# Performance work log

Hardware: AMD Instinct MI355X
Metric: run time of the kernel (lower is better)

Reference implementation:

```python
import jax, jax.numpy as jnp
import numpy as np

C = 256
HEADS = 8
HEAD_DIM = C // HEADS
SCALE = HEAD_DIM ** -0.5
POOL = 2
LN_EPS = 1e-5


def setup_inputs() -> dict:
    key = jax.random.key(0)
    ks = jax.random.split(key, 10)
    B, H, W = 8, 64, 64
    std = 0.02
    return {
        "x": jax.random.normal(ks[0], (B, C, H, W), jnp.float32),
        "Wq": jax.random.normal(ks[1], (HEADS, C), jnp.float32) * std,
        "Wk": jax.random.normal(ks[2], (HEADS, C), jnp.float32) * std,
        "Wv": jax.random.normal(ks[3], (C, C), jnp.float32) * std,
        "Wsr": jax.random.normal(ks[4], (C, C), jnp.float32) * (2.0 / C) ** 0.5,
        "bsr": jnp.zeros((C,), jnp.float32),
        "gamma": jnp.ones((C,), jnp.float32),
        "beta": jnp.zeros((C,), jnp.float32),
        "Wp": jax.random.normal(ks[5], (C, C), jnp.float32) * std,
        "bp": jnp.zeros((C,), jnp.float32),
    }


def reference(x, Wq, Wk, Wv, Wsr, bsr, gamma, beta, Wp, bp):
    B, Cc, H, W = x.shape
    N = H * W
    # tokens [B, N, C]
    tok = x.reshape(B, Cc, N).transpose(0, 2, 1)
    # q: Linear(C -> heads), per-head scalar query  [B, heads, N]
    q = jnp.einsum("bnc,hc->bhn", tok, Wq)
    # spatial reduction: avgpool(pool_ratio) then 1x1 conv
    xp = x.reshape(B, Cc, H // POOL, POOL, W // POOL, POOL).mean(axis=(3, 5))
    xs = jnp.einsum("bchw,oc->bohw", xp, Wsr) + bsr[None, :, None, None]
    M = (H // POOL) * (W // POOL)
    x_ = xs.reshape(B, Cc, M).transpose(0, 2, 1)  # [B, M, C]
    # LayerNorm + GELU (exact erf, torch default)
    mu = x_.mean(-1, keepdims=True)
    var = ((x_ - mu) ** 2).mean(-1, keepdims=True)
    x_ = (x_ - mu) * jax.lax.rsqrt(var + LN_EPS) * gamma + beta
    x_ = jax.nn.gelu(x_, approximate=False)
    # k: per-head scalar key [B, heads, M]; v: [B, heads, M, head_dim]
    k = jnp.einsum("bmc,hc->bhm", x_, Wk)
    v = jnp.einsum("bmc,oc->bmo", x_, Wv).reshape(B, M, HEADS, HEAD_DIM).transpose(0, 2, 1, 3)
    # rank-1 attention scores [B, heads, N, M]
    attn = jax.nn.softmax(q[:, :, :, None] * k[:, :, None, :] * SCALE, axis=-1)
    out = jnp.einsum("bhnm,bhmd->bhnd", attn, v)  # [B, heads, N, head_dim]
    out = out.transpose(0, 2, 1, 3).reshape(B, N, Cc)
    out = out @ Wp.T + bp
    return out.transpose(0, 2, 1).reshape(B, Cc, H, W)
```

## Files before the change

### kernel.cpp

```cpp
#include <hip/hip_runtime.h>
#include <math.h>


#define NH 8
#define NJ 8
#define NT (NH * NJ)
#define SCALE 0.17677669529663687f

__device__ __constant__ float INVFACT[NJ] = {
    1.0f, 1.0f, 0.5f, 1.6666666666666666e-01f, 4.1666666666666664e-02f,
    8.3333333333333332e-03f, 1.3888888888888889e-03f, 1.9841269841269841e-04f};

__global__ void k0_q_prep(const float* __restrict__ x, const float* __restrict__ Wq,
                          const float* __restrict__ Wsr, const float* __restrict__ Wv,
                          float* __restrict__ q01, float* __restrict__ WsrT,
                          float* __restrict__ WvT) {
    __shared__ float wq[NH * 128];
    const int tid = threadIdx.x;
    const int blk = blockIdx.x;
    if (blk < 256) {
        const int b = blk >> 5, half = (blk >> 4) & 1, nt = blk & 15;
#pragma unroll
        for (int r = 0; r < 4; ++r) {
            int idx = r * 256 + tid;
            int h = idx >> 7, cc = idx & 127;
            wq[idx] = Wq[h * 256 + half * 128 + cc];
        }
        __syncthreads();
        const int n = nt * 256 + tid;
        const float* xb = x + (((size_t)b << 8) + half * 128) * 4096 + n;
        float acc[NH] = {};
#pragma unroll 8
        for (int c = 0; c < 128; ++c) {
            float xv = xb[(size_t)c << 12];
#pragma unroll
            for (int h = 0; h < NH; ++h) acc[h] += xv * wq[h * 128 + c];
        }
#pragma unroll
        for (int h = 0; h < NH; ++h)
            q01[((size_t)(half * 64 + b * 8 + h) << 12) + n] = acc[h];
    } else {
        const float* W = (blk < 288) ? Wsr : Wv;
        float* WT = (blk < 288) ? WsrT : WvT;
        const int c0 = (blk & 31) * 8;
#pragma unroll
        for (int r = 0; r < 2; ++r) {
            int fidx = r * 256 + tid;
            int c = c0 + (fidx >> 6), o4 = (fidx & 63) * 4;
            float4 t;
            t.x = W[(size_t)(o4 + 0) * 256 + c];
            t.y = W[(size_t)(o4 + 1) * 256 + c];
            t.z = W[(size_t)(o4 + 2) * 256 + c];
            t.w = W[(size_t)(o4 + 3) * 256 + c];
            *(float4*)&WT[(size_t)c * 256 + o4] = t;
        }
    }
}

__global__ void ka_mega(const float* __restrict__ x, const float* __restrict__ WsrT,
                        const float* __restrict__ bsr, const float* __restrict__ WvT,
                        const float* __restrict__ gamma, const float* __restrict__ beta,
                        const float* __restrict__ Wk,
                        float* __restrict__ v, float* __restrict__ kout) {
    __shared__ float smem[20352];
    float* a_pool = smem;
    float* wpan   = smem + 1152;
    float* g_lds  = smem + 9472;
    float4* wkv   = (float4*)(smem + 17792);
    float4* glv   = (float4*)(smem + 19840);
    float4* blv   = (float4*)(smem + 20096);

    const int tid = threadIdx.x;
    const int blk = blockIdx.x;
    const int b = blk >> 5, mt = blk & 31;
    const int m0 = mt * 32;
    const int i2 = mt;

    const int ccs = tid >> 3, jg = tid & 7;
    const int mg = tid & 7, og = tid >> 3;

    const float4* Wk4 = (const float4*)Wk;
    wkv[tid] = Wk4[tid];
    wkv[256 + tid] = Wk4[256 + tid];
    if (tid < 64) {
        glv[tid] = ((const float4*)gamma)[tid];
        blv[tid] = ((const float4*)beta)[tid];
    }

    float acc[4][8] = {};
    for (int c0 = 0; c0 < 256; c0 += 32) {
        __syncthreads();
        {
            const float* p = x + ((size_t)(b * 256 + c0 + ccs) << 12) +
                             i2 * 128 + jg * 8;
            float4 r00 = *(const float4*)p;
            float4 r01 = *(const float4*)(p + 4);
            float4 r10 = *(const float4*)(p + 64);
            float4 r11 = *(const float4*)(p + 68);
            float4 pv;
            pv.x = 0.25f * ((r00.x + r00.y) + (r10.x + r10.y));
            pv.y = 0.25f * ((r00.z + r00.w) + (r10.z + r10.w));
            pv.z = 0.25f * ((r01.x + r01.y) + (r11.x + r11.y));
            pv.w = 0.25f * ((r01.z + r01.w) + (r11.z + r11.w));
            *(float4*)&a_pool[ccs * 36 + jg * 4] = pv;
        }
#pragma unroll
        for (int r = 0; r < 8; ++r) {
            int fidx = r * 256 + tid;
            int cc = fidx >> 6, o4 = (fidx & 63) * 4;
            *(float4*)&wpan[cc * 260 + o4] =
                *(const float4*)&WsrT[(size_t)(c0 + cc) * 256 + o4];
        }
        __syncthreads();
#pragma unroll
        for (int cc = 0; cc < 32; ++cc) {
            float4 av = *(const float4*)&a_pool[cc * 36 + mg * 4];
            float4 b0 = *(const float4*)&wpan[cc * 260 + og * 8];
            float4 b1 = *(const float4*)&wpan[cc * 260 + og * 8 + 4];
            float am[4] = {av.x, av.y, av.z, av.w};
            float bo[8] = {b0.x, b0.y, b0.z, b0.w, b1.x, b1.y, b1.z, b1.w};
#pragma unroll
            for (int i = 0; i < 4; ++i)
#pragma unroll
                for (int j = 0; j < 8; ++j) acc[i][j] += am[i] * bo[j];
        }
    }
    {
        float4 bs0 = *(const float4*)&bsr[og * 8];
        float4 bs1 = *(const float4*)&bsr[og * 8 + 4];
#pragma unroll
        for (int i = 0; i < 4; ++i) {
            float4 w0, w1;
            w0.x = acc[i][0] + bs0.x; w0.y = acc[i][1] + bs0.y;
            w0.z = acc[i][2] + bs0.z; w0.w = acc[i][3] + bs0.w;
            w1.x = acc[i][4] + bs1.x; w1.y = acc[i][5] + bs1.y;
            w1.z = acc[i][6] + bs1.z; w1.w = acc[i][7] + bs1.w;
            *(float4*)&g_lds[(mg * 4 + i) * 260 + og * 8] = w0;
            *(float4*)&g_lds[(mg * 4 + i) * 260 + og * 8 + 4] = w1;
        }
    }
    __syncthreads();

    const int wave = tid >> 6, lane = tid & 63;
    const float4 g4 = glv[lane], be4 = blv[lane];
#pragma unroll
    for (int ti = 0; ti < 8; ++ti) {
        const int mm = wave * 8 + ti;
        float4 vv = *(const float4*)&g_lds[mm * 260 + lane * 4];
        float s = (vv.x + vv.y) + (vv.z + vv.w);
        float s2 = (vv.x * vv.x + vv.y * vv.y) + (vv.z * vv.z + vv.w * vv.w);
#pragma unroll
        for (int off = 1; off < 64; off <<= 1) {
            s += __shfl_xor(s, off);
            s2 += __shfl_xor(s2, off);
        }
        const float mu = s * (1.f / 256.f);
        const float rstd = rsqrtf(s2 * (1.f / 256.f) - mu * mu + 1e-5f);
        float4 gg;
        {
            float xh;
            xh = (vv.x - mu) * rstd * g4.x + be4.x;
            gg.x = 0.5f * xh * (1.f + erff(xh * 0.70710678118654752f));
            xh = (vv.y - mu) * rstd * g4.y + be4.y;
            gg.y = 0.5f * xh * (1.f + erff(xh * 0.70710678118654752f));
            xh = (vv.z - mu) * rstd * g4.z + be4.z;
            gg.z = 0.5f * xh * (1.f + erff(xh * 0.70710678118654752f));
            xh = (vv.w - mu) * rstd * g4.w + be4.w;
            gg.w = 0.5f * xh * (1.f + erff(xh * 0.70710678118654752f));
        }
        *(float4*)&g_lds[mm * 260 + lane * 4] = gg;
        float acck[NH];
#pragma unroll
        for (int h = 0; h < NH; ++h) {
            float4 w = wkv[h * 64 + lane];
            acck[h] = (gg.x * w.x + gg.y * w.y) + (gg.z * w.z + gg.w * w.w);
        }
#pragma unroll
        for (int off = 1; off < 64; off <<= 1)
#pragma unroll
            for (int h = 0; h < NH; ++h) acck[h] += __shfl_xor(acck[h], off);
        if (lane == 0) {
#pragma unroll
            for (int h = 0; h < NH; ++h)
                kout[((size_t)(b * 8 + h) << 10) + m0 + mm] = acck[h];
        }
    }

    float accv[4][8] = {};
    for (int c0 = 0; c0 < 256; c0 += 32) {
        __syncthreads();
#pragma unroll
        for (int r = 0; r < 8; ++r) {
            int fidx = r * 256 + tid;
            int cc = fidx >> 6, o4 = (fidx & 63) * 4;
            *(float4*)&wpan[cc * 260 + o4] =
                *(const float4*)&WvT[(size_t)(c0 + cc) * 256 + o4];
        }
        __syncthreads();
#pragma unroll
        for (int cc = 0; cc < 32; ++cc) {
            const int c = c0 + cc;
            float a0 = g_lds[(mg * 4 + 0) * 260 + c];
            float a1 = g_lds[(mg * 4 + 1) * 260 + c];
            float a2 = g_lds[(mg * 4 + 2) * 260 + c];
            float a3 = g_lds[(mg * 4 + 3) * 260 + c];
            float4 b0 = *(const float4*)&wpan[cc * 260 + og * 8];
            float4 b1 = *(const float4*)&wpan[cc * 260 + og * 8 + 4];
            float bo[8] = {b0.x, b0.y, b0.z, b0.w, b1.x, b1.y, b1.z, b1.w};
#pragma unroll
            for (int j = 0; j < 8; ++j) {
                accv[0][j] += a0 * bo[j];
                accv[1][j] += a1 * bo[j];
                accv[2][j] += a2 * bo[j];
                accv[3][j] += a3 * bo[j];
            }
        }
    }
#pragma unroll
    for (int i = 0; i < 4; ++i) {
        float4 r0, r1;
        r0.x = accv[i][0]; r0.y = accv[i][1]; r0.z = accv[i][2]; r0.w = accv[i][3];
        r1.x = accv[i][4]; r1.y = accv[i][5]; r1.z = accv[i][6]; r1.w = accv[i][7];
        float* dst = &v[((size_t)(b << 10) + m0 + mg * 4 + i) * 256 + og * 8];
        *(float4*)dst = r0;
        *(float4*)(dst + 4) = r1;
    }
}

__global__ void kc_moments_project(const float* __restrict__ kin,
                                   const float* __restrict__ v,
                                   const float* __restrict__ Wp,
                                   float* __restrict__ P, float* __restrict__ S2) {
    const int bh = blockIdx.x;
    const int h = bh & 7, b = bh >> 3;
    const int tid = threadIdx.x;
    const int g = tid >> 5, d = tid & 31;
    float accM[NJ] = {};
    float accS[NJ] = {};
    const float* kb = kin + ((size_t)bh << 10);
    const float* vb = v + ((size_t)b << 18) + h * 32 + d;
#pragma unroll 4
    for (int mi = 0; mi < 128; ++mi) {
        int m = g * 128 + mi;
        float km = kb[m];
        float w = vb[(size_t)m << 8];
        float t = w, ts = 1.f;
#pragma unroll
        for (int j = 0; j < NJ; ++j) {
            accM[j] += t;
            accS[j] += ts;
            t *= km;
            ts *= km;
        }
    }
    __shared__ float red[8][NJ][33];
#pragma unroll
    for (int j = 0; j < NJ; ++j) red[g][j][d] = accM[j];
    if (d == 0) {
#pragma unroll
        for (int j = 0; j < NJ; ++j) red[g][j][32] = accS[j];
    }
    __syncthreads();
    __shared__ float Ms[NJ][33];
    for (int idx = tid; idx < NJ * 33; idx += 256) {
        int j = idx / 33, dd = idx % 33;
        float sum = 0.f;
#pragma unroll
        for (int gg = 0; gg < 8; ++gg) sum += red[gg][j][dd];
        Ms[j][dd] = sum * INVFACT[j];
    }
    __syncthreads();
    const int c = tid;
    float wp[32];
    const float* wrow = Wp + c * 256 + h * 32;
#pragma unroll
    for (int i = 0; i < 8; ++i) {
        float4 t = *(const float4*)(wrow + i * 4);
        wp[i * 4 + 0] = t.x; wp[i * 4 + 1] = t.y;
        wp[i * 4 + 2] = t.z; wp[i * 4 + 3] = t.w;
    }
#pragma unroll
    for (int j = 0; j < NJ; ++j) {
        float s = 0.f;
#pragma unroll
        for (int dd = 0; dd < 32; ++dd) s += wp[dd] * Ms[j][dd];
        P[((size_t)bh * NJ + j) * 256 + c] = s;
    }
    if (tid < NJ) S2[bh * NJ + tid] = Ms[tid][32];
}

__global__ void kd_out(const float* __restrict__ q01, const float* __restrict__ S2,
                       const float* __restrict__ P, const float* __restrict__ bp,
                       float* __restrict__ out) {
    __shared__ float p_lds[NT * 264];
    __shared__ float coef_lds[NT * 32];
    __shared__ float s2l[NT];
    const int tid = threadIdx.x;
    const int b = blockIdx.x >> 7, nt = blockIdx.x & 127;
    const int n0 = nt * 32;
    if (tid < NT) s2l[tid] = S2[b * NT + tid];
    const float* Pb = P + (size_t)b * (NT * 256);
#pragma unroll
    for (int r = 0; r < 16; ++r) {
        int fidx = r * 256 + tid;
        int t = fidx >> 6, c4 = (fidx & 63) * 4;
        *(float4*)&p_lds[t * 264 + c4] = *(const float4*)&Pb[t * 256 + c4];
    }
    __syncthreads();
    {
        const int n = tid & 31, h = tid >> 5;
        size_t qi = ((size_t)(b * NH + h) << 12) + n0 + n;
        float a = (q01[qi] + q01[qi + ((size_t)64 << 12)]) * SCALE;
        float den = s2l[h * NJ + NJ - 1];
#pragma unroll
        for (int j = NJ - 2; j >= 0; --j) den = den * a + s2l[h * NJ + j];
        float p = 1.0f / den;
#pragma unroll
        for (int j = 0; j < NJ; ++j) {
            coef_lds[(h * NJ + j) * 32 + n] = p;
            p *= a;
        }
    }
    __syncthreads();
    const int ng = tid & 7, og = tid >> 3;
    float acc[8][4] = {};
#pragma unroll 8
    for (int t = 0; t < NT; ++t) {
        float4 nv = *(const float4*)&coef_lds[t * 32 + ng * 4];
        float4 cv0 = *(const float4*)&p_lds[t * 264 + og * 8];
        float4 cv1 = *(const float4*)&p_lds[t * 264 + og * 8 + 4];
        float nm[4] = {nv.x, nv.y, nv.z, nv.w};
        float cm[8] = {cv0.x, cv0.y, cv0.z, cv0.w, cv1.x, cv1.y, cv1.z, cv1.w};
#pragma unroll
        for (int i = 0; i < 8; ++i)
#pragma unroll
            for (int j = 0; j < 4; ++j) acc[i][j] += cm[i] * nm[j];
    }
    float* ob = out + ((size_t)(b << 8) + og * 8) * 4096 + n0 + ng * 4;
#pragma unroll
    for (int i = 0; i < 8; ++i) {
        float bpc = bp[og * 8 + i];
        float4 r;
        r.x = acc[i][0] + bpc; r.y = acc[i][1] + bpc;
        r.z = acc[i][2] + bpc; r.w = acc[i][3] + bpc;
        *(float4*)(ob + (size_t)i * 4096) = r;
    }
}

extern "C" void kernel_launch(void* const* d_in, const int* in_sizes, int n_in,
                              void* d_out, int out_size, void* d_ws, size_t ws_size,
                              hipStream_t stream) {
    const float* x     = (const float*)d_in[0];
    const float* Wq    = (const float*)d_in[1];
    const float* Wk    = (const float*)d_in[2];
    const float* Wv    = (const float*)d_in[3];
    const float* Wsr   = (const float*)d_in[4];
    const float* bsr   = (const float*)d_in[5];
    const float* gamma = (const float*)d_in[6];
    const float* beta  = (const float*)d_in[7];
    const float* Wp    = (const float*)d_in[8];
    const float* bp    = (const float*)d_in[9];
    float* out = (float*)d_out;

    float* ws   = (float*)d_ws;
    float* vbuf = ws;
    float* q01  = vbuf + 2097152;
    float* kbuf = q01 + 524288;
    float* P    = kbuf + 65536;
    float* S2   = P + 131072;
    float* WsrT = S2 + 512;
    float* WvT  = WsrT + 65536;

    k0_q_prep<<<320, 256, 0, stream>>>(x, Wq, Wsr, Wv, q01, WsrT, WvT);
    ka_mega<<<256, 256, 0, stream>>>(x, WsrT, bsr, WvT, gamma, beta, Wk,
                                     vbuf, kbuf);
    kc_moments_project<<<64, 256, 0, stream>>>(kbuf, vbuf, Wp, P, S2);
    kd_out<<<1024, 256, 0, stream>>>(q01, S2, P, bp, out);
}
```

Before: 206.8 us.

## Double-buffer weight panels via registers and swizzle LDS tiles in ka_mega

Restructures ka_mega so all pooled inputs are computed up front into a swizzled LDS tile. Both GEMM stages now stream weight panels through a register-staged double buffer, which removes one barrier per iteration and overlaps global loads with FMAs. The GELU output is also written transposed and swizzled, so the second GEMM reads float4 vectors instead of scalar strided loads. LDS use rises to about 140KB with launch_bounds(256,1), which limits each CU to one block and raises register pressure.

```diff
diff --git a/kernel.cpp b/kernel.cpp
--- a/kernel.cpp
+++ b/kernel.cpp
@@ -57,18 +57,19 @@
     }
 }
 
-__global__ void ka_mega(const float* __restrict__ x, const float* __restrict__ WsrT,
-                        const float* __restrict__ bsr, const float* __restrict__ WvT,
-                        const float* __restrict__ gamma, const float* __restrict__ beta,
-                        const float* __restrict__ Wk,
-                        float* __restrict__ v, float* __restrict__ kout) {
-    __shared__ float smem[20352];
-    float* a_pool = smem;
-    float* wpan   = smem + 1152;
-    float* g_lds  = smem + 9472;
-    float4* wkv   = (float4*)(smem + 17792);
-    float4* glv   = (float4*)(smem + 19840);
-    float4* blv   = (float4*)(smem + 20096);
+__global__ __launch_bounds__(256, 1) void ka_mega(
+        const float* __restrict__ x, const float* __restrict__ WsrT,
+        const float* __restrict__ bsr, const float* __restrict__ WvT,
+        const float* __restrict__ gamma, const float* __restrict__ beta,
+        const float* __restrict__ Wk,
+        float* __restrict__ v, float* __restrict__ kout) {
+    __shared__ __attribute__((aligned(16))) float smem[35456];
+    float* wpan  = smem;
+    float* gsh   = smem + 16384;
+    float* g_t   = smem + 24704;
+    float4* wkv  = (float4*)(smem + 32896);
+    float4* glv  = (float4*)(smem + 34944);
+    float4* blv  = (float4*)(smem + 35200);
 
     const int tid = threadIdx.x;
     const int blk = blockIdx.x;
@@ -76,56 +77,74 @@
     const int m0 = mt * 32;
     const int i2 = mt;
 
-    const int ccs = tid >> 3, jg = tid & 7;
     const int mg = tid & 7, og = tid >> 3;
 
-    const float4* Wk4 = (const float4*)Wk;
-    wkv[tid] = Wk4[tid];
-    wkv[256 + tid] = Wk4[256 + tid];
-    if (tid < 64) {
-        glv[tid] = ((const float4*)gamma)[tid];
-        blv[tid] = ((const float4*)beta)[tid];
-    }
-
-    float acc[4][8] = {};
-    for (int c0 = 0; c0 < 256; c0 += 32) {
-        __syncthreads();
-        {
-            const float* p = x + ((size_t)(b * 256 + c0 + ccs) << 12) +
-                             i2 * 128 + jg * 8;
-            float4 r00 = *(const float4*)p;
-            float4 r01 = *(const float4*)(p + 4);
-            float4 r10 = *(const float4*)(p + 64);
-            float4 r11 = *(const float4*)(p + 68);
+    {
+        const int ccs = tid >> 3, jg = tid & 7;
+        const int pcb = (jg * 4) ^ (((ccs >> 2) & 7) << 2);
+#pragma unroll 2
+        for (int p = 0; p < 8; ++p) {
+            const int c = p * 32 + ccs;
+            const float* px = x + ((size_t)(b * 256 + c) << 12) + i2 * 128 + jg * 8;
+            float4 r00 = *(const float4*)px;
+            float4 r01 = *(const float4*)(px + 4);
+            float4 r10 = *(const float4*)(px + 64);
+            float4 r11 = *(const float4*)(px + 68);
             float4 pv;
             pv.x = 0.25f * ((r00.x + r00.y) + (r10.x + r10.y));
             pv.y = 0.25f * ((r00.z + r00.w) + (r10.z + r10.w));
             pv.z = 0.25f * ((r01.x + r01.y) + (r11.x + r11.y));
             pv.w = 0.25f * ((r01.z + r01.w) + (r11.z + r11.w));
-            *(float4*)&a_pool[ccs * 36 + jg * 4] = pv;
-        }
-#pragma unroll
-        for (int r = 0; r < 8; ++r) {
-            int fidx = r * 256 + tid;
-            int cc = fidx >> 6, o4 = (fidx & 63) * 4;
-            *(float4*)&wpan[cc * 260 + o4] =
-                *(const float4*)&WsrT[(size_t)(c0 + cc) * 256 + o4];
-        }
-        __syncthreads();
-#pragma unroll
-        for (int cc = 0; cc < 32; ++cc) {
-            float4 av = *(const float4*)&a_pool[cc * 36 + mg * 4];
-            float4 b0 = *(const float4*)&wpan[cc * 260 + og * 8];
-            float4 b1 = *(const float4*)&wpan[cc * 260 + og * 8 + 4];
-            float am[4] = {av.x, av.y, av.z, av.w};
-            float bo[8] = {b0.x, b0.y, b0.z, b0.w, b1.x, b1.y, b1.z, b1.w};
-#pragma unroll
-            for (int i = 0; i < 4; ++i)
-#pragma unroll
-                for (int j = 0; j < 8; ++j) acc[i][j] += am[i] * bo[j];
-        }
-    }
-    {
+            *(float4*)&gsh[(c << 5) + pcb] = pv;
+        }
+    }
+    {
+        const float4* src = (const float4*)WsrT;
+#pragma unroll
+        for (int r = 0; r < 8; ++r)
+            *(float4*)&wpan[(r * 256 + tid) * 4] = src[r * 256 + tid];
+    }
+    {
+        const float4* Wk4 = (const float4*)Wk;
+        wkv[tid] = Wk4[tid];
+        wkv[256 + tid] = Wk4[256 + tid];
+        if (tid < 64) {
+            glv[tid] = ((const float4*)gamma)[tid];
+            blv[tid] = ((const float4*)beta)[tid];
+        }
+    }
+    __syncthreads();
+
+    float4 wreg[8];
+    {
+        float acc[4][8] = {};
+        for (int p = 0; p < 8; ++p) {
+            if (p < 7) {
+                const float4* src = (const float4*)(WsrT + ((size_t)(p + 1) << 13));
+#pragma unroll
+                for (int r = 0; r < 8; ++r) wreg[r] = src[r * 256 + tid];
+            }
+            const float* wp = wpan + ((p & 1) << 13);
+#pragma unroll
+            for (int cc = 0; cc < 32; ++cc) {
+                const int swzc = ((cc >> 2) & 7) << 2;
+                float4 av = *(const float4*)&gsh[((p * 32 + cc) << 5) + ((mg << 2) ^ swzc)];
+                float4 b0 = *(const float4*)&wp[cc * 256 + og * 8];
+                float4 b1 = *(const float4*)&wp[cc * 256 + og * 8 + 4];
+                float am[4] = {av.x, av.y, av.z, av.w};
+                float bo[8] = {b0.x, b0.y, b0.z, b0.w, b1.x, b1.y, b1.z, b1.w};
+#pragma unroll
+                for (int i = 0; i < 4; ++i)
+#pragma unroll
+                    for (int j = 0; j < 8; ++j) acc[i][j] += am[i] * bo[j];
+            }
+            if (p < 7) {
+#pragma unroll
+                for (int r = 0; r < 8; ++r)
+                    *(float4*)&wpan[(((p + 1) & 1) << 13) + (r * 256 + tid) * 4] = wreg[r];
+            }
+            __syncthreads();
+        }
         float4 bs0 = *(const float4*)&bsr[og * 8];
         float4 bs1 = *(const float4*)&bsr[og * 8 + 4];
 #pragma unroll
@@ -135,86 +154,115 @@
             w0.z = acc[i][2] + bs0.z; w0.w = acc[i][3] + bs0.w;
             w1.x = acc[i][4] + bs1.x; w1.y = acc[i][5] + bs1.y;
             w1.z = acc[i][6] + bs1.z; w1.w = acc[i][7] + bs1.w;
-            *(float4*)&g_lds[(mg * 4 + i) * 260 + og * 8] = w0;
-            *(float4*)&g_lds[(mg * 4 + i) * 260 + og * 8 + 4] = w1;
+            *(float4*)&gsh[(mg * 4 + i) * 260 + og * 8] = w0;
+            *(float4*)&gsh[(mg * 4 + i) * 260 + og * 8 + 4] = w1;
         }
     }
     __syncthreads();
 
     const int wave = tid >> 6, lane = tid & 63;
-    const float4 g4 = glv[lane], be4 = blv[lane];
-#pragma unroll
-    for (int ti = 0; ti < 8; ++ti) {
-        const int mm = wave * 8 + ti;
-        float4 vv = *(const float4*)&g_lds[mm * 260 + lane * 4];
-        float s = (vv.x + vv.y) + (vv.z + vv.w);
-        float s2 = (vv.x * vv.x + vv.y * vv.y) + (vv.z * vv.z + vv.w * vv.w);
-#pragma unroll
-        for (int off = 1; off < 64; off <<= 1) {
-            s += __shfl_xor(s, off);
-            s2 += __shfl_xor(s2, off);
-        }
-        const float mu = s * (1.f / 256.f);
-        const float rstd = rsqrtf(s2 * (1.f / 256.f) - mu * mu + 1e-5f);
-        float4 gg;
+    {
+        const float4 g4 = glv[lane], be4 = blv[lane];
+        float4 wkreg[NH];
+#pragma unroll
+        for (int h = 0; h < NH; ++h) wkreg[h] = wkv[h * 64 + lane];
         {
-            float xh;
-            xh = (vv.x - mu) * rstd * g4.x + be4.x;
-            gg.x = 0.5f * xh * (1.f + erff(xh * 0.70710678118654752f));
-            xh = (vv.y - mu) * rstd * g4.y + be4.y;
-            gg.y = 0.5f * xh * (1.f + erff(xh * 0.70710678118654752f));
-            xh = (vv.z - mu) * rstd * g4.z + be4.z;
-            gg.z = 0.5f * xh * (1.f + erff(xh * 0.70710678118654752f));
-            xh = (vv.w - mu) * rstd * g4.w + be4.w;
-            gg.w = 0.5f * xh * (1.f + erff(xh * 0.70710678118654752f));
-        }
-        *(float4*)&g_lds[mm * 260 + lane * 4] = gg;
-        float acck[NH];
-#pragma unroll
-        for (int h = 0; h < NH; ++h) {
-            float4 w = wkv[h * 64 + lane];
-            acck[h] = (gg.x * w.x + gg.y * w.y) + (gg.z * w.z + gg.w * w.w);
-        }
-#pragma unroll
-        for (int off = 1; off < 64; off <<= 1)
-#pragma unroll
-            for (int h = 0; h < NH; ++h) acck[h] += __shfl_xor(acck[h], off);
-        if (lane == 0) {
-#pragma unroll
-            for (int h = 0; h < NH; ++h)
-                kout[((size_t)(b * 8 + h) << 10) + m0 + mm] = acck[h];
-        }
-    }
+            const float4* src = (const float4*)WvT;
+#pragma unroll
+            for (int r = 0; r < 8; ++r) wreg[r] = src[r * 256 + tid];
+        }
+        float4 gg4[8];
+#pragma unroll
+        for (int ti = 0; ti < 8; ++ti) {
+            const int mm = wave * 8 + ti;
+            float4 vv = *(const float4*)&gsh[mm * 260 + lane * 4];
+            float s = (vv.x + vv.y) + (vv.z + vv.w);
+            float s2 = (vv.x * vv.x + vv.y * vv.y) + (vv.z * vv.z + vv.w * vv.w);
+#pragma unroll
+            for (int off = 1; off < 64; off <<= 1) {
+                s += __shfl_xor(s, off);
+                s2 += __shfl_xor(s2, off);
+            }
+            const float mu = s * (1.f / 256.f);
+            const float rstd = rsqrtf(s2 * (1.f / 256.f) - mu * mu + 1e-5f);
+            float4 gg;
+            {
+                float xh;
+                xh = (vv.x - mu) * rstd * g4.x + be4.x;
+                gg.x = 0.5f * xh * (1.f + erff(xh * 0.70710678118654752f));
+                xh = (vv.y - mu) * rstd * g4.y + be4.y;
+                gg.y = 0.5f * xh * (1.f + erff(xh * 0.70710678118654752f));
+                xh = (vv.z - mu) * rstd * g4.z + be4.z;
+                gg.z = 0.5f * xh * (1.f + erff(xh * 0.70710678118654752f));
+                xh = (vv.w - mu) * rstd * g4.w + be4.w;
+                gg.w = 0.5f * xh * (1.f + erff(xh * 0.70710678118654752f));
+            }
+            gg4[ti] = gg;
+            float acck[NH];
+#pragma unroll
+            for (int h = 0; h < NH; ++h) {
+                float4 w = wkreg[h];
+                acck[h] = (gg.x * w.x + gg.y * w.y) + (gg.z * w.z + gg.w * w.w);
+            }
+#pragma unroll
+            for (int off = 1; off < 64; off <<= 1)
+#pragma unroll
+                for (int h = 0; h < NH; ++h) acck[h] += __shfl_xor(acck[h], off);
+            if (lane == 0) {
+#pragma unroll
+                for (int h = 0; h < NH; ++h)
+                    kout[((size_t)(b * 8 + h) << 10) + m0 + mm] = acck[h];
+            }
+        }
+        {
+            const int s = lane & 7;
+            const int cb0 = ((wave ^ (s >> 1)) << 3) | ((s & 1) << 2);
+            const int cb1 = cb0 ^ 4;
+            const int r0 = (lane * 4) << 5;
+            float4 t;
+#define GT_WRITE(K, COMP)                                                   \
+            t.x = gg4[0].COMP; t.y = gg4[1].COMP;                           \
+            t.z = gg4[2].COMP; t.w = gg4[3].COMP;                           \
+            *(float4*)&g_t[r0 + ((K) << 5) + cb0] = t;                      \
+            t.x = gg4[4].COMP; t.y = gg4[5].COMP;                           \
+            t.z = gg4[6].COMP; t.w = gg4[7].COMP;                           \
+            *(float4*)&g_t[r0 + ((K) << 5) + cb1] = t;
+            GT_WRITE(0, x) GT_WRITE(1, y) GT_WRITE(2, z) GT_WRITE(3, w)
+#undef GT_WRITE
+        }
+#pragma unroll
+        for (int r = 0; r < 8; ++r)
+            *(float4*)&wpan[(r * 256 + tid) * 4] = wreg[r];
+    }
+    __syncthreads();
 
     float accv[4][8] = {};
-    for (int c0 = 0; c0 < 256; c0 += 32) {
+    for (int p = 0; p < 8; ++p) {
+        if (p < 7) {
+            const float4* src = (const float4*)(WvT + ((size_t)(p + 1) << 13));
+#pragma unroll
+            for (int r = 0; r < 8; ++r) wreg[r] = src[r * 256 + tid];
+        }
+        const float* wp = wpan + ((p & 1) << 13);
+#pragma unroll
+        for (int cc = 0; cc < 32; ++cc) {
+            const int swzc = ((cc >> 2) & 7) << 2;
+            float4 av = *(const float4*)&g_t[((p * 32 + cc) << 5) + ((mg << 2) ^ swzc)];
+            float4 b0 = *(const float4*)&wp[cc * 256 + og * 8];
+            float4 b1 = *(const float4*)&wp[cc * 256 + og * 8 + 4];
+            float am[4] = {av.x, av.y, av.z, av.w};
+            float bo[8] = {b0.x, b0.y, b0.z, b0.w, b1.x, b1.y, b1.z, b1.w};
+#pragma unroll
+            for (int i = 0; i < 4; ++i)
+#pragma unroll
+                for (int j = 0; j < 8; ++j) accv[i][j] += am[i] * bo[j];
+        }
+        if (p < 7) {
+#pragma unroll
+            for (int r = 0; r < 8; ++r)
+                *(float4*)&wpan[(((p + 1) & 1) << 13) + (r * 256 + tid) * 4] = wreg[r];
+        }
         __syncthreads();
-#pragma unroll
-        for (int r = 0; r < 8; ++r) {
-            int fidx = r * 256 + tid;
-            int cc = fidx >> 6, o4 = (fidx & 63) * 4;
-            *(float4*)&wpan[cc * 260 + o4] =
-                *(const float4*)&WvT[(size_t)(c0 + cc) * 256 + o4];
-        }
-        __syncthreads();
-#pragma unroll
-        for (int cc = 0; cc < 32; ++cc) {
-            const int c = c0 + cc;
-            float a0 = g_lds[(mg * 4 + 0) * 260 + c];
-            float a1 = g_lds[(mg * 4 + 1) * 260 + c];
-            float a2 = g_lds[(mg * 4 + 2) * 260 + c];
-            float a3 = g_lds[(mg * 4 + 3) * 260 + c];
-            float4 b0 = *(const float4*)&wpan[cc * 260 + og * 8];
-            float4 b1 = *(const float4*)&wpan[cc * 260 + og * 8 + 4];
-            float bo[8] = {b0.x, b0.y, b0.z, b0.w, b1.x, b1.y, b1.z, b1.w};
-#pragma unroll
-            for (int j = 0; j < 8; ++j) {
-                accv[0][j] += a0 * bo[j];
-                accv[1][j] += a1 * bo[j];
-                accv[2][j] += a2 * bo[j];
-                accv[3][j] += a3 * bo[j];
-            }
-        }
     }
 #pragma unroll
     for (int i = 0; i < 4; ++i) {
```

After: 237.6 us. 1.15x slower.
